# Performance work log

Measured on AMD Instinct MI355X. Metric: run time of the kernel, lower is better.

The kernel has to match this reference:

```python
import jax, jax.numpy as jnp
import numpy as np

C = 256
RED = 2
C2 = C // RED


def setup_inputs() -> dict:
    key = jax.random.key(0)
    ks = jax.random.split(key, 6)
    B, H, W = 8, 64, 64
    x = jax.random.normal(ks[0], (B, C, H, W), dtype=jnp.float32)
    # 1x1 convs stored as [out_ch, in_ch] matrices
    W1 = jax.random.normal(ks[1], (C2, C), dtype=jnp.float32) * (1.0 / np.sqrt(C))
    b1 = jax.random.normal(ks[2], (C2,), dtype=jnp.float32) * 0.01
    W2 = jax.random.normal(ks[3], (C, C2), dtype=jnp.float32) * (1.0 / np.sqrt(C2))
    b2 = jax.random.normal(ks[4], (C,), dtype=jnp.float32) * 0.01
    # torch inits scale to zeros; use randn so the residual branch is active
    scale = jax.random.normal(ks[5], (1, C, 1, 1), dtype=jnp.float32)
    return {"x": x, "W1": W1, "b1": b1, "W2": W2, "b2": b2, "scale": scale}


def reference(x, W1, b1, W2, b2, scale):
    B, Cc, H, Wd = x.shape
    # conv1 (1x1): [B,C,H,W] -> [B,C2,H,W]
    y = jnp.einsum('bchw,oc->bohw', x, W1) + b1[None, :, None, None]
    # flatten spatial, move channels last: [B, N, C2]
    y = y.reshape(B, C2, H * Wd).transpose(0, 2, 1)
    # unscaled self-attention over N spatial positions
    att = jax.nn.softmax(jnp.einsum('bmc,bnc->bmn', y, y), axis=-1)  # [B,N,N]
    out = jnp.einsum('bmn,bnc->bmc', att, y)  # [B,N,C2]
    # faithful to torch: raw .view(B,-1,H,W) WITHOUT permuting back
    out = out.reshape(B, C2, H, Wd)
    # conv2 (1x1): [B,C2,H,W] -> [B,C,H,W]
    out = jnp.einsum('bchw,oc->bohw', out, W2) + b2[None, :, None, None]
    return out * scale + x
```

## Files before the change

### kernel.cpp

```cpp
#include <hip/hip_runtime.h>

#define B_  8
#define C_  256
#define C2_ 128
#define N_  4096
#define LOG2E 1.44269504088896f

typedef _Float16 f16;
typedef _Float16 f16x2 __attribute__((ext_vector_type(2)));
typedef _Float16 f16x8 __attribute__((ext_vector_type(8)));
typedef float f32x4  __attribute__((ext_vector_type(4)));

static __device__ __forceinline__ unsigned pk2(float a, float b) {
  f16x2 h = {(f16)a, (f16)b};
  return __builtin_bit_cast(unsigned, h);
}

__global__ __launch_bounds__(256)
void prep_kernel(const float* __restrict__ W1, const float* __restrict__ W2,
                 f16* __restrict__ w1h, f16* __restrict__ w2h)
{
  int i = blockIdx.x * 256 + threadIdx.x;
  w1h[i] = (f16)W1[i];
  w2h[i] = (f16)W2[i];
}

__global__ __launch_bounds__(256, 3)
void conv1_kernel(const float* __restrict__ x,
                  const f16* __restrict__ w1h,
                  const float* __restrict__ b1,
                  f16* __restrict__ Y, f16* __restrict__ Yt)
{
  __shared__ __align__(16) char smem[49152];
  float* Xr = (float*)smem;
  f16*   Ah = (f16*)(smem + 32768);
  f16*   T  = (f16*)smem;

  const int t = threadIdx.x;
  const int w = t >> 6, lane = t & 63, quad = lane >> 4, l16 = lane & 15;
  const int b = blockIdx.x, nt0 = blockIdx.y;

#pragma unroll
  for (int pass = 0; pass < 8; pass++) {
    int c  = (t >> 3) + pass * 32;
    int n4 = t & 7;
    float4 v = *(const float4*)(x + ((long)(b * C_ + c)) * N_ + nt0 * 32 + n4 * 4);
    *(float4*)(&Xr[c * 32 + (n4 ^ (c & 7)) * 4]) = v;
  }
  __syncthreads();
#pragma unroll
  for (int pass = 0; pass < 4; pass++) {
    int n  = t & 31;
    int kb = (t >> 5) + pass * 8;
    f16x8 vh;
#pragma unroll
    for (int jj = 0; jj < 8; jj++) {
      int cc = kb * 8 + jj;
      vh[jj] = (f16)Xr[cc * 32 + ((n >> 2) ^ (cc & 7)) * 4 + (n & 3)];
    }
    *(f16x8*)(&Ah[n * 256 + (kb ^ (n & 7)) * 8]) = vh;
  }
  __syncthreads();

  f16x8 bh[2][8];
#pragma unroll
  for (int nt = 0; nt < 2; nt++) {
    int c2 = w * 32 + nt * 16 + l16;
#pragma unroll
    for (int ks = 0; ks < 8; ks++)
      bh[nt][ks] = *(const f16x8*)(w1h + c2 * C_ + ks * 32 + quad * 8);
  }

  f32x4 acc[2][2];
#pragma unroll
  for (int i = 0; i < 2; i++)
#pragma unroll
    for (int j = 0; j < 2; j++) acc[i][j] = (f32x4){0.f, 0.f, 0.f, 0.f};

#pragma unroll
  for (int ks = 0; ks < 8; ks++)
#pragma unroll
    for (int mt = 0; mt < 2; mt++) {
      f16x8 ah = *(const f16x8*)(&Ah[(mt * 16 + l16) * 256 + (((ks * 4 + quad) ^ (l16 & 7))) * 8]);
#pragma unroll
      for (int nt = 0; nt < 2; nt++)
        acc[mt][nt] = __builtin_amdgcn_mfma_f32_16x16x32_f16(ah, bh[nt][ks], acc[mt][nt], 0, 0, 0);
    }
  __syncthreads();

#pragma unroll
  for (int nt = 0; nt < 2; nt++) {
    int c2 = w * 32 + nt * 16 + l16;
    float bv = b1[c2];
#pragma unroll
    for (int mt = 0; mt < 2; mt++)
#pragma unroll
      for (int rg = 0; rg < 4; rg++) {
        int n = mt * 16 + quad * 4 + rg;
        T[c2 * 40 + n] = (f16)(acc[mt][nt][rg] + bv);
      }
  }
  __syncthreads();
#pragma unroll
  for (int pass = 0; pass < 2; pass++) {
    int r  = (t >> 2) + pass * 64;
    int c8 = (t & 3) * 8;
    f16x8 v = *(const f16x8*)(&T[r * 40 + c8]);
    *(f16x8*)(Yt + ((long)(b * C2_ + r)) * N_ + nt0 * 32 + c8) = v;
  }
#pragma unroll
  for (int pass = 0; pass < 2; pass++) {
    int row = t & 31;
    int cg  = (t >> 5) + pass * 8;
    f16x8 v;
#pragma unroll
    for (int jj = 0; jj < 8; jj++) v[jj] = T[(cg * 8 + jj) * 40 + row];
    *(f16x8*)(Y + ((long)(b * N_ + nt0 * 32 + row)) * C2_ + cg * 8) = v;
  }
}

__global__ __launch_bounds__(256, 2)
void attn_kernel(const f16* __restrict__ Y, const f16* __restrict__ Yt,
                 f16* __restrict__ Op, float* __restrict__ ls)
{
  __shared__ f16 Ks[64 * 128];
  __shared__ f16 Vs[128 * 64];
  __shared__ float nsqf[128];

  const int t = threadIdx.x;
  const int w = t >> 6, lane = t & 63, quad = lane >> 4, l16 = lane & 15;
  const int b = blockIdx.x, qt = blockIdx.y, s = blockIdx.z;
  const f16* Yb  = Y  + (long)b * N_ * C2_;
  const f16* Ytb = Yt + (long)b * C2_ * N_;
  const int kbase0 = s * 2048;

  f16x8 qf[2][4];
#pragma unroll
  for (int mt = 0; mt < 2; mt++)
#pragma unroll
    for (int ks = 0; ks < 4; ks++)
      qf[mt][ks] = *(const f16x8*)(Yb + (long)(qt * 128 + w * 32 + mt * 16 + l16) * C2_ + ks * 32 + quad * 8);

  {
    int r = t >> 1, half = t & 1;
    float ss = 0.f;
#pragma unroll
    for (int j = 0; j < 8; j++) {
      f16x8 v = *(const f16x8*)(Yb + (long)(qt * 128 + r) * C2_ + half * 64 + j * 8);
#pragma unroll
      for (int e = 0; e < 8; e++) { float f = (float)v[e]; ss = fmaf(f, f, ss); }
    }
    ss += __shfl_xor(ss, 1);
    if (!half) nsqf[r] = ss;
  }

#pragma unroll
  for (int pass = 0; pass < 4; pass++) {
    int r = (t >> 4) + pass * 16;
    f16x8 kv = *(const f16x8*)(Yb + (long)(kbase0 + r) * C2_ + (t & 15) * 8);
    *(f16x8*)(&Ks[r * 128 + (((t & 15)) ^ (r & 15)) * 8]) = kv;
  }
#pragma unroll
  for (int pass = 0; pass < 4; pass++) {
    int d = (t >> 3) + pass * 32;
    f16x8 vv = *(const f16x8*)(Ytb + (long)d * N_ + kbase0 + (t & 7) * 8);
    *(f16x8*)(&Vs[d * 64 + (((t & 7)) ^ (d & 7)) * 8]) = vv;
  }
  __syncthreads();

  float nm[2];
  nm[0] = nsqf[w * 32 + l16] * LOG2E;
  nm[1] = nsqf[w * 32 + 16 + l16] * LOG2E;

  f16x8 ones8;
#pragma unroll
  for (int j = 0; j < 8; j++) ones8[j] = (f16)1.0f;

  f32x4 Oa[2][8];
#pragma unroll
  for (int i = 0; i < 2; i++)
#pragma unroll
    for (int j = 0; j < 8; j++) Oa[i][j] = (f32x4){0.f, 0.f, 0.f, 0.f};
  f32x4 lac[2] = {(f32x4){0.f,0.f,0.f,0.f}, (f32x4){0.f,0.f,0.f,0.f}};

#pragma unroll 1
  for (int kt = 0; kt < 32; kt++) {
    f16x8 stK[4], stV[4];
    if (kt + 1 < 32) {
      int nb = kbase0 + (kt + 1) * 64;
#pragma unroll
      for (int pass = 0; pass < 4; pass++)
        stK[pass] = *(const f16x8*)(Yb + (long)(nb + (t >> 4) + pass * 16) * C2_ + (t & 15) * 8);
#pragma unroll
      for (int pass = 0; pass < 4; pass++)
        stV[pass] = *(const f16x8*)(Ytb + (long)((t >> 3) + pass * 32) * N_ + nb + (t & 7) * 8);
    }

    f32x4 S[4][2];
#pragma unroll
    for (int i = 0; i < 4; i++)
#pragma unroll
      for (int j = 0; j < 2; j++) S[i][j] = (f32x4){0.f, 0.f, 0.f, 0.f};
#pragma unroll
    for (int ks = 0; ks < 4; ks++) {
      f16x8 bfr[4];
#pragma unroll
      for (int nt = 0; nt < 4; nt++)
        bfr[nt] = *(const f16x8*)(&Ks[(nt * 16 + l16) * 128 + (((ks * 4 + quad) ^ l16)) * 8]);
#pragma unroll
      for (int nt = 0; nt < 4; nt++)
#pragma unroll
        for (int mt = 0; mt < 2; mt++)
          S[nt][mt] = __builtin_amdgcn_mfma_f32_16x16x32_f16(bfr[nt], qf[mt][ks], S[nt][mt], 0, 0, 0);
    }

    unsigned Xp[2][4][2];
#pragma unroll
    for (int mt = 0; mt < 2; mt++)
#pragma unroll
      for (int nt = 0; nt < 4; nt++) {
        float p0 = exp2f(fminf(fmaf(S[nt][mt][0], LOG2E, -nm[mt]), 11.0f));
        float p1 = exp2f(fminf(fmaf(S[nt][mt][1], LOG2E, -nm[mt]), 11.0f));
        float p2 = exp2f(fminf(fmaf(S[nt][mt][2], LOG2E, -nm[mt]), 11.0f));
        float p3 = exp2f(fminf(fmaf(S[nt][mt][3], LOG2E, -nm[mt]), 11.0f));
        Xp[mt][nt][0] = pk2(p0, p1);
        Xp[mt][nt][1] = pk2(p2, p3);
      }

    f16x8 pa[2][2];
    {
      const bool par = (quad & 1) != 0;
#pragma unroll
      for (int mt = 0; mt < 2; mt++) {
#pragma unroll
        for (int pr = 0; pr < 2; pr++)
#pragma unroll
          for (int d = 0; d < 2; d++) {
            auto r = __builtin_amdgcn_permlane32_swap(Xp[mt][2 * pr][d], Xp[mt][2 * pr + 1][d], false, false);
            Xp[mt][2 * pr][d]     = r[0];
            Xp[mt][2 * pr + 1][d] = r[1];
          }
#pragma unroll
        for (int ks2 = 0; ks2 < 2; ks2++) {
          unsigned lo0 = Xp[mt][2 * ks2][0],     lo1 = Xp[mt][2 * ks2][1];
          unsigned hi0 = Xp[mt][2 * ks2 + 1][0], hi1 = Xp[mt][2 * ks2 + 1][1];
          unsigned lo0x = (unsigned)__builtin_amdgcn_ds_swizzle((int)lo0, 0x401F);
          unsigned lo1x = (unsigned)__builtin_amdgcn_ds_swizzle((int)lo1, 0x401F);
          unsigned hi0x = (unsigned)__builtin_amdgcn_ds_swizzle((int)hi0, 0x401F);
          unsigned hi1x = (unsigned)__builtin_amdgcn_ds_swizzle((int)hi1, 0x401F);
          union { unsigned u[4]; f16x8 v; } P;
          P.u[0] = par ? hi0x : lo0;
          P.u[1] = par ? hi1x : lo1;
          P.u[2] = par ? hi0  : lo0x;
          P.u[3] = par ? hi1  : lo1x;
          pa[ks2][mt] = P.v;
        }
      }
    }

#pragma unroll
    for (int ks2 = 0; ks2 < 2; ks2++) {
      f16x8 vb[8];
#pragma unroll
      for (int dt = 0; dt < 8; dt++)
        vb[dt] = *(const f16x8*)(&Vs[(dt * 16 + l16) * 64 + (((ks2 * 4 + quad) ^ (l16 & 7))) * 8]);
#pragma unroll
      for (int mt = 0; mt < 2; mt++) {
#pragma unroll
        for (int dt = 0; dt < 8; dt++)
          Oa[mt][dt] = __builtin_amdgcn_mfma_f32_16x16x32_f16(pa[ks2][mt], vb[dt], Oa[mt][dt], 0, 0, 0);
        lac[mt] = __builtin_amdgcn_mfma_f32_16x16x32_f16(pa[ks2][mt], ones8, lac[mt], 0, 0, 0);
      }
    }

    __syncthreads();
    if (kt + 1 < 32) {
#pragma unroll
      for (int pass = 0; pass < 4; pass++) {
        int r = (t >> 4) + pass * 16;
        *(f16x8*)(&Ks[r * 128 + (((t & 15)) ^ (r & 15)) * 8]) = stK[pass];
      }
#pragma unroll
      for (int pass = 0; pass < 4; pass++) {
        int d = (t >> 3) + pass * 32;
        *(f16x8*)(&Vs[d * 64 + (((t & 7)) ^ (d & 7)) * 8]) = stV[pass];
      }
    }
    __syncthreads();
  }

  const long rbase = ((long)s * B_ + b) * N_ + qt * 128;
#pragma unroll
  for (int mt = 0; mt < 2; mt++)
#pragma unroll
    for (int rg = 0; rg < 4; rg++) {
      int r = w * 32 + mt * 16 + quad * 4 + rg;
#pragma unroll
      for (int dt = 0; dt < 8; dt++)
        Op[(rbase + r) * C2_ + dt * 16 + l16] = (f16)Oa[mt][dt][rg];
      if (l16 == 0) ls[rbase + r] = lac[mt][rg];
    }
}

__global__ __launch_bounds__(256, 4)
void conv2_kernel(const f16* __restrict__ Op, const float* __restrict__ ls,
                  const f16* __restrict__ w2h,
                  const float* __restrict__ b2,
                  const float* __restrict__ scale,
                  const float* __restrict__ x,
                  float* __restrict__ out)
{
  __shared__ f16 Or[128 * 72];
  __shared__ f16 Bsw[64 * 128];
  __shared__ float invL[128];

  const int t = threadIdx.x;
  const int w = t >> 6, lane = t & 63, quad = lane >> 4, l16 = lane & 15;
  const int b = blockIdx.x, pt = blockIdx.y, oh = blockIdx.z;
  const long base0 = (long)b * 524288;
  const long base1 = 4194304 + base0;

  if (t < 128) {
    int q = t * 32 + (pt >> 1);
    float l = ls[(long)b * N_ + q] + ls[32768 + (long)b * N_ + q];
    invL[t] = 1.0f / fmaxf(l, 1e-20f);
  }
  __syncthreads();

#pragma unroll
  for (int pass = 0; pass < 4; pass++) {
    int j = (t >> 3) + pass * 32;
    int c8 = (t & 7) * 8;
    f16x8 a0 = *(const f16x8*)(Op + base0 + (long)j * N_ + pt * 64 + c8);
    f16x8 a1 = *(const f16x8*)(Op + base1 + (long)j * N_ + pt * 64 + c8);
    float iv = invL[j];
    f16x8 r;
#pragma unroll
    for (int jj = 0; jj < 8; jj++)
      r[jj] = (f16)(((float)a0[jj] + (float)a1[jj]) * iv);
    *(f16x8*)(&Or[j * 72 + c8]) = r;
  }
  __syncthreads();
#pragma unroll
  for (int pass = 0; pass < 4; pass++) {
    int p = t & 63;
    int q = (t >> 6) + pass * 4;
    f16x8 vv;
#pragma unroll
    for (int jj = 0; jj < 8; jj++) vv[jj] = Or[(q * 8 + jj) * 72 + p];
    *(f16x8*)(&Bsw[p * 128 + ((q ^ (p & 15))) * 8]) = vv;
  }
  __syncthreads();

  f32x4 acc[2][4];
#pragma unroll
  for (int i = 0; i < 2; i++)
#pragma unroll
    for (int j = 0; j < 4; j++) acc[i][j] = (f32x4){0.f, 0.f, 0.f, 0.f};

#pragma unroll
  for (int ks = 0; ks < 4; ks++) {
    f16x8 bfr[4];
#pragma unroll
    for (int nt = 0; nt < 4; nt++)
      bfr[nt] = *(const f16x8*)(&Bsw[(nt * 16 + l16) * 128 + (((ks * 4 + quad) ^ l16)) * 8]);
#pragma unroll
    for (int mt = 0; mt < 2; mt++) {
      int o = oh * 128 + w * 32 + mt * 16 + l16;
      f16x8 ah = *(const f16x8*)(w2h + o * C2_ + ks * 32 + quad * 8);
#pragma unroll
      for (int nt = 0; nt < 4; nt++)
        acc[mt][nt] = __builtin_amdgcn_mfma_f32_16x16x32_f16(ah, bfr[nt], acc[mt][nt], 0, 0, 0);
    }
  }
#pragma unroll
  for (int mt = 0; mt < 2; mt++)
#pragma unroll
    for (int rg = 0; rg < 4; rg++) {
      int o = oh * 128 + w * 32 + mt * 16 + quad * 4 + rg;
      float so = scale[o], bo = b2[o];
#pragma unroll
      for (int nt = 0; nt < 4; nt++) {
        int p = pt * 64 + nt * 16 + l16;
        long xo = ((long)b * C_ + o) * N_ + p;
        out[xo] = (acc[mt][nt][rg] + bo) * so + x[xo];
      }
    }
}

extern "C" void kernel_launch(void* const* d_in, const int* in_sizes, int n_in,
                              void* d_out, int out_size, void* d_ws, size_t ws_size,
                              hipStream_t stream) {
  const float* x     = (const float*)d_in[0];
  const float* W1    = (const float*)d_in[1];
  const float* b1    = (const float*)d_in[2];
  const float* W2    = (const float*)d_in[3];
  const float* b2    = (const float*)d_in[4];
  const float* scale = (const float*)d_in[5];
  float* outp = (float*)d_out;

  const size_t NE = (size_t)B_ * N_ * C2_;
  f16* Y   = (f16*)d_ws;
  f16* Yt  = Y + NE;
  f16* Op  = Yt + NE;
  float* ls = (float*)(Op + 2 * NE);
  f16* w1h = (f16*)(ls + 65536);
  f16* w2h = w1h + 32768;

  prep_kernel <<<dim3(128),      dim3(256), 0, stream>>>(W1, W2, w1h, w2h);
  conv1_kernel<<<dim3(8, 128),   dim3(256), 0, stream>>>(x, w1h, b1, Y, Yt);
  attn_kernel <<<dim3(8, 32, 2), dim3(256), 0, stream>>>(Y, Yt, Op, ls);
  conv2_kernel<<<dim3(8, 64, 2), dim3(256), 0, stream>>>(Op, ls, w2h, b2, scale, x, outp);
}
```

Before: 213.1 us.

## Generalize attention key split to up to four partitions and raise occupancy

The attention kernel now splits the key range into a runtime-chosen number of partitions (up to four, if workspace allows) instead of a fixed two. This raises the grid from 512 to as many as 1024 blocks to better fill the GPU's compute units, and launch bounds are raised to 4 blocks per SIMD-group occupancy target. conv2 now sums a variable number of partial outputs and normalizers, which adds global memory traffic. The f16 packing also switches to the cvt_pkrtz intrinsic, which uses round-toward-zero.

Result: slower. 449.7 us (+111.0%).

```diff
diff --git a/kernel.cpp b/kernel.cpp
--- a/kernel.cpp
+++ b/kernel.cpp
@@ -7,13 +7,11 @@
 #define LOG2E 1.44269504088896f
 
 typedef _Float16 f16;
-typedef _Float16 f16x2 __attribute__((ext_vector_type(2)));
 typedef _Float16 f16x8 __attribute__((ext_vector_type(8)));
 typedef float f32x4  __attribute__((ext_vector_type(4)));
 
 static __device__ __forceinline__ unsigned pk2(float a, float b) {
-  f16x2 h = {(f16)a, (f16)b};
-  return __builtin_bit_cast(unsigned, h);
+  return __builtin_bit_cast(unsigned, __builtin_amdgcn_cvt_pkrtz(a, b));
 }
 
 __global__ __launch_bounds__(256)
@@ -119,7 +117,7 @@
   }
 }
 
-__global__ __launch_bounds__(256, 2)
+__global__ __launch_bounds__(256, 4)
 void attn_kernel(const f16* __restrict__ Y, const f16* __restrict__ Yt,
                  f16* __restrict__ Op, float* __restrict__ ls)
 {
@@ -130,9 +128,11 @@
   const int t = threadIdx.x;
   const int w = t >> 6, lane = t & 63, quad = lane >> 4, l16 = lane & 15;
   const int b = blockIdx.x, qt = blockIdx.y, s = blockIdx.z;
+  const int ns = gridDim.z;
   const f16* Yb  = Y  + (long)b * N_ * C2_;
   const f16* Ytb = Yt + (long)b * C2_ * N_;
-  const int kbase0 = s * 2048;
+  const int g0 = (s * 64) / ns;
+  const int g1 = ((s + 1) * 64) / ns;
 
   f16x8 qf[2][4];
 #pragma unroll
@@ -154,17 +154,20 @@
     if (!half) nsqf[r] = ss;
   }
 
-#pragma unroll
-  for (int pass = 0; pass < 4; pass++) {
-    int r = (t >> 4) + pass * 16;
-    f16x8 kv = *(const f16x8*)(Yb + (long)(kbase0 + r) * C2_ + (t & 15) * 8);
-    *(f16x8*)(&Ks[r * 128 + (((t & 15)) ^ (r & 15)) * 8]) = kv;
-  }
-#pragma unroll
-  for (int pass = 0; pass < 4; pass++) {
-    int d = (t >> 3) + pass * 32;
-    f16x8 vv = *(const f16x8*)(Ytb + (long)d * N_ + kbase0 + (t & 7) * 8);
-    *(f16x8*)(&Vs[d * 64 + (((t & 7)) ^ (d & 7)) * 8]) = vv;
+  {
+    const int kb0 = g0 * 64;
+#pragma unroll
+    for (int pass = 0; pass < 4; pass++) {
+      int r = (t >> 4) + pass * 16;
+      f16x8 kv = *(const f16x8*)(Yb + (long)(kb0 + r) * C2_ + (t & 15) * 8);
+      *(f16x8*)(&Ks[r * 128 + (((t & 15)) ^ (r & 15)) * 8]) = kv;
+    }
+#pragma unroll
+    for (int pass = 0; pass < 4; pass++) {
+      int d = (t >> 3) + pass * 32;
+      f16x8 vv = *(const f16x8*)(Ytb + (long)d * N_ + kb0 + (t & 7) * 8);
+      *(f16x8*)(&Vs[d * 64 + (((t & 7)) ^ (d & 7)) * 8]) = vv;
+    }
   }
   __syncthreads();
 
@@ -184,10 +187,10 @@
   f32x4 lac[2] = {(f32x4){0.f,0.f,0.f,0.f}, (f32x4){0.f,0.f,0.f,0.f}};
 
 #pragma unroll 1
-  for (int kt = 0; kt < 32; kt++) {
+  for (int g = g0; g < g1; g++) {
     f16x8 stK[4], stV[4];
-    if (kt + 1 < 32) {
-      int nb = kbase0 + (kt + 1) * 64;
+    if (g + 1 < g1) {
+      int nb = (g + 1) * 64;
 #pragma unroll
       for (int pass = 0; pass < 4; pass++)
         stK[pass] = *(const f16x8*)(Yb + (long)(nb + (t >> 4) + pass * 16) * C2_ + (t & 15) * 8);
@@ -274,7 +277,7 @@
     }
 
     __syncthreads();
-    if (kt + 1 < 32) {
+    if (g + 1 < g1) {
 #pragma unroll
       for (int pass = 0; pass < 4; pass++) {
         int r = (t >> 4) + pass * 16;
@@ -308,7 +311,7 @@
                   const float* __restrict__ b2,
                   const float* __restrict__ scale,
                   const float* __restrict__ x,
-                  float* __restrict__ out)
+                  float* __restrict__ out, int ns)
 {
   __shared__ f16 Or[128 * 72];
   __shared__ f16 Bsw[64 * 128];
@@ -318,11 +321,12 @@
   const int w = t >> 6, lane = t & 63, quad = lane >> 4, l16 = lane & 15;
   const int b = blockIdx.x, pt = blockIdx.y, oh = blockIdx.z;
   const long base0 = (long)b * 524288;
-  const long base1 = 4194304 + base0;
 
   if (t < 128) {
     int q = t * 32 + (pt >> 1);
-    float l = ls[(long)b * N_ + q] + ls[32768 + (long)b * N_ + q];
+    float l = 0.f;
+    for (int si = 0; si < ns; si++)
+      l += ls[(long)si * 32768 + (long)b * N_ + q];
     invL[t] = 1.0f / fmaxf(l, 1e-20f);
   }
   __syncthreads();
@@ -331,13 +335,17 @@
   for (int pass = 0; pass < 4; pass++) {
     int j = (t >> 3) + pass * 32;
     int c8 = (t & 7) * 8;
-    f16x8 a0 = *(const f16x8*)(Op + base0 + (long)j * N_ + pt * 64 + c8);
-    f16x8 a1 = *(const f16x8*)(Op + base1 + (long)j * N_ + pt * 64 + c8);
+    float fa[8] = {0.f,0.f,0.f,0.f,0.f,0.f,0.f,0.f};
+    for (int si = 0; si < ns; si++) {
+      f16x8 a = *(const f16x8*)(Op + (long)si * 4194304 + base0 + (long)j * N_ + pt * 64 + c8);
+#pragma unroll
+      for (int jj = 0; jj < 8; jj++) fa[jj] += (float)a[jj];
+    }
     float iv = invL[j];
     f16x8 r;
 #pragma unroll
     for (int jj = 0; jj < 8; jj++)
-      r[jj] = (f16)(((float)a0[jj] + (float)a1[jj]) * iv);
+      r[jj] = (f16)(fa[jj] * iv);
     *(f16x8*)(&Or[j * 72 + c8]) = r;
   }
   __syncthreads();
@@ -400,15 +408,23 @@
   float* outp = (float*)d_out;
 
   const size_t NE = (size_t)B_ * N_ * C2_;
+
+  int ns = 4;
+  while (ns > 2) {
+    size_t need = (size_t)(2 + ns) * NE * 2 + (size_t)ns * (B_ * N_ * 4) + 131072;
+    if (need <= ws_size) break;
+    ns--;
+  }
+
   f16* Y   = (f16*)d_ws;
   f16* Yt  = Y + NE;
   f16* Op  = Yt + NE;
-  float* ls = (float*)(Op + 2 * NE);
-  f16* w1h = (f16*)(ls + 65536);
+  float* ls = (float*)(Op + (size_t)ns * NE);
+  f16* w1h = (f16*)(ls + (size_t)ns * 32768);
   f16* w2h = w1h + 32768;
 
-  prep_kernel <<<dim3(128),      dim3(256), 0, stream>>>(W1, W2, w1h, w2h);
-  conv1_kernel<<<dim3(8, 128),   dim3(256), 0, stream>>>(x, w1h, b1, Y, Yt);
-  attn_kernel <<<dim3(8, 32, 2), dim3(256), 0, stream>>>(Y, Yt, Op, ls);
-  conv2_kernel<<<dim3(8, 64, 2), dim3(256), 0, stream>>>(Op, ls, w2h, b2, scale, x, outp);
-}
+  prep_kernel <<<dim3(128),       dim3(256), 0, stream>>>(W1, W2, w1h, w2h);
+  conv1_kernel<<<dim3(8, 128),    dim3(256), 0, stream>>>(x, w1h, b1, Y, Yt);
+  attn_kernel <<<dim3(8, 32, ns), dim3(256), 0, stream>>>(Y, Yt, Op, ls);
+  conv2_kernel<<<dim3(8, 64, 2),  dim3(256), 0, stream>>>(Op, ls, w2h, b2, scale, x, outp, ns);
+}
```
